# Performance work log

Measured on AMD Instinct MI355X. Metric: run time of the kernel, lower is better.

The kernel has to match this reference:

```python
import jax, jax.numpy as jnp
import numpy as np

N = 8192   # nodes
F = 16     # node features (col 0 = signal, last 3 = xyz)
H = 64     # hidden
G = 256    # number of graphs (segments)
EPS = 1e-3 # keras LayerNormalization default epsilon


def setup_inputs() -> dict:
    key = jax.random.key(0)
    ks = jax.random.split(key, 10)
    s = 0.05
    X = jax.random.normal(ks[0], (N, F), jnp.float32)
    # dense pre-normalized adjacency (spektral GCNConv expects normalized A)
    A = jax.random.uniform(ks[1], (N, N), jnp.float32) * (1.0 / N)
    I = jnp.sort(jax.random.randint(ks[2], (N,), 0, G)).astype(jnp.int32)
    W0 = jax.random.normal(ks[3], (F, H), jnp.float32) * s
    b0 = jnp.zeros((H,), jnp.float32)
    g0 = jnp.ones((H,), jnp.float32)
    be0 = jnp.zeros((H,), jnp.float32)
    W1 = jax.random.normal(ks[4], (H, H), jnp.float32) * s
    b1 = jnp.zeros((H,), jnp.float32)
    g1 = jnp.ones((H,), jnp.float32)
    be1 = jnp.zeros((H,), jnp.float32)
    Wf = jax.random.normal(ks[5], (H, H), jnp.float32) * s
    bf = jnp.zeros((H,), jnp.float32)
    Wa = jax.random.normal(ks[6], (H, H), jnp.float32) * s
    ba = jnp.zeros((H,), jnp.float32)
    Wout = jax.random.normal(ks[7], (H + 3, 3), jnp.float32) * s
    bout = jnp.zeros((3,), jnp.float32)
    return dict(X=X, A=A, I=I, W0=W0, b0=b0, g0=g0, be0=be0,
                W1=W1, b1=b1, g1=g1, be1=be1,
                Wf=Wf, bf=bf, Wa=Wa, ba=ba, Wout=Wout, bout=bout)


def _layer_norm(x, gamma, beta):
    m = jnp.mean(x, axis=-1, keepdims=True)
    v = jnp.mean(jnp.square(x - m), axis=-1, keepdims=True)
    return (x - m) * jax.lax.rsqrt(v + EPS) * gamma + beta


def reference(X, A, I, W0, b0, g0, be0, W1, b1, g1, be1, Wf, bf, Wa, ba, Wout, bout):
    I = I.astype(jnp.int32)
    # GCN layer 0: relu(A @ X @ W0 + b0) -> LayerNorm
    h0 = _layer_norm(jax.nn.relu(A @ (X @ W0) + b0), g0, be0)
    # GCN layer 1 + LayerNorm + residual (i > 0)
    h = _layer_norm(jax.nn.relu(A @ (h0 @ W1) + b1), g1, be1) + h0
    # GlobalAttentionPool: Dense features * sigmoid-gated attention, segment-summed per graph
    feat = h @ Wf + bf                       # [N, H]
    attn = jax.nn.sigmoid(h @ Wa + ba)       # [N, H]
    g = jax.ops.segment_sum(feat * attn, I, num_segments=G)  # [G, H]
    # Signal-weighted barycentre via segment-softmax over log1p(relu(signal))
    z = jnp.log1p(jax.nn.relu(X[:, 0]))                       # [N]
    zmax = jax.ops.segment_max(z, I, num_segments=G)          # [G]
    zexp = jnp.exp(z - zmax[I])                               # [N]
    zsum = jax.ops.segment_sum(zexp, I, num_segments=G)       # [G]
    w = zexp / zsum[I]                                        # [N]
    bary = jax.ops.segment_sum(w[:, None] * X[:, -3:], I, num_segments=G)  # [G, 3]
    return jnp.concatenate([g, bary], axis=-1) @ Wout + bout  # [G, 3]
```

## Files before the change

kernel.cpp:

```cpp
#include <hip/hip_runtime.h>
#include <hip/hip_bf16.h>
#include <math.h>

#define NN 8192
#define FF 16
#define HH 64
#define GG 256
#define LN_EPS 1e-3f
#define KSPLIT 8
#define KC (NN / KSPLIT)

typedef __bf16 bf16x8 __attribute__((ext_vector_type(8)));
typedef float  floatx4 __attribute__((ext_vector_type(4)));

__global__ void k1_xw0(const float* __restrict__ X,
                       const float* __restrict__ W0,
                       const int* __restrict__ I,
                       __hip_bfloat16* __restrict__ Zt0,
                       float* __restrict__ zarr,
                       unsigned int* __restrict__ zmax_bits) {
    const int b = blockIdx.x, tid = threadIdx.x;
    const int lane = tid & 63;
    const int i = (b & 127) * 64 + lane;
    const int n = ((b >> 7) << 2) + (tid >> 6);
    float s = 0.f;
#pragma unroll
    for (int m = 0; m < FF; ++m)
        s += X[i * FF + m] * W0[m * HH + n];
    Zt0[(size_t)n * NN + i] = __float2bfloat16(s);

    if (b < 128 && tid < 64) {
        const int ii = b * 64 + lane;
        float z = log1pf(fmaxf(X[ii * FF], 0.f));
        zarr[ii] = z;
        atomicMax(&zmax_bits[I[ii]], __float_as_uint(z));
    }
}

__global__ __launch_bounds__(256)
void k_gemm_split(const float* __restrict__ A,
                  const __hip_bfloat16* __restrict__ Zt,
                  float* __restrict__ C) {
    const int tid  = threadIdx.x;
    const int wave = tid >> 6;
    const int lane = tid & 63;
    const int l16  = lane & 15;
    const int quad = lane >> 4;
    const int rb   = blockIdx.x & 127;
    const int kb   = blockIdx.x >> 7;
    const int row0 = rb * 64;
    const int k0   = kb * KC;

    const float* aptr = A + (size_t)(row0 + wave * 16 + l16) * NN + k0 + quad * 8;
    const __hip_bfloat16* bp0 = Zt + (size_t)(0 * 16 + l16) * NN + k0 + quad * 8;
    const __hip_bfloat16* bp1 = Zt + (size_t)(1 * 16 + l16) * NN + k0 + quad * 8;
    const __hip_bfloat16* bp2 = Zt + (size_t)(2 * 16 + l16) * NN + k0 + quad * 8;
    const __hip_bfloat16* bp3 = Zt + (size_t)(3 * 16 + l16) * NN + k0 + quad * 8;

    floatx4 acc0 = {0.f,0.f,0.f,0.f}, acc1 = {0.f,0.f,0.f,0.f};
    floatx4 acc2 = {0.f,0.f,0.f,0.f}, acc3 = {0.f,0.f,0.f,0.f};

#pragma unroll 4
    for (int k = 0; k < KC; k += 32) {
        const float4 a0 = *reinterpret_cast<const float4*>(aptr + k);
        const float4 a1 = *reinterpret_cast<const float4*>(aptr + k + 4);
        bf16x8 af;
        af[0] = (__bf16)a0.x; af[1] = (__bf16)a0.y;
        af[2] = (__bf16)a0.z; af[3] = (__bf16)a0.w;
        af[4] = (__bf16)a1.x; af[5] = (__bf16)a1.y;
        af[6] = (__bf16)a1.z; af[7] = (__bf16)a1.w;
        const bf16x8 b0 = *reinterpret_cast<const bf16x8*>(bp0 + k);
        const bf16x8 b1 = *reinterpret_cast<const bf16x8*>(bp1 + k);
        const bf16x8 b2 = *reinterpret_cast<const bf16x8*>(bp2 + k);
        const bf16x8 b3 = *reinterpret_cast<const bf16x8*>(bp3 + k);
        acc0 = __builtin_amdgcn_mfma_f32_16x16x32_bf16(af, b0, acc0, 0, 0, 0);
        acc1 = __builtin_amdgcn_mfma_f32_16x16x32_bf16(af, b1, acc1, 0, 0, 0);
        acc2 = __builtin_amdgcn_mfma_f32_16x16x32_bf16(af, b2, acc2, 0, 0, 0);
        acc3 = __builtin_amdgcn_mfma_f32_16x16x32_bf16(af, b3, acc3, 0, 0, 0);
    }

    const size_t rbase = (size_t)(row0 + wave * 16 + quad * 4);
#pragma unroll
    for (int r = 0; r < 4; ++r) {
        float* crow = C + (rbase + r) * HH + l16;
        atomicAdd(crow +  0, acc0[r]);
        atomicAdd(crow + 16, acc1[r]);
        atomicAdd(crow + 32, acc2[r]);
        atomicAdd(crow + 48, acc3[r]);
    }
}

__global__ __launch_bounds__(256)
void k_ln(const float* __restrict__ C,
          const float* __restrict__ bias,
          const float* __restrict__ gamma,
          const float* __restrict__ beta,
          const float* __restrict__ resid,
          float* __restrict__ out) {
    const int tid = threadIdx.x;
    const int row = tid >> 4;
    const int c0  = (tid & 15) * 4;
    const size_t grow = (size_t)(blockIdx.x * 16 + row);

    float4 v4 = *reinterpret_cast<const float4*>(&C[grow * HH + c0]);
    const float4 b4 = *reinterpret_cast<const float4*>(&bias[c0]);
    float v[4] = { fmaxf(v4.x + b4.x, 0.f), fmaxf(v4.y + b4.y, 0.f),
                   fmaxf(v4.z + b4.z, 0.f), fmaxf(v4.w + b4.w, 0.f) };
    float s = 0.f, ss = 0.f;
#pragma unroll
    for (int j = 0; j < 4; ++j) { s += v[j]; ss += v[j] * v[j]; }
#pragma unroll
    for (int m = 1; m < 16; m <<= 1) {
        s  += __shfl_xor(s,  m, 64);
        ss += __shfl_xor(ss, m, 64);
    }
    const float mean = s * (1.f / 64.f);
    const float var  = fmaxf(ss * (1.f / 64.f) - mean * mean, 0.f);
    const float inv  = rsqrtf(var + LN_EPS);
    const float4 g4  = *reinterpret_cast<const float4*>(&gamma[c0]);
    const float4 be4 = *reinterpret_cast<const float4*>(&beta[c0]);
    float4 o;
    o.x = (v[0] - mean) * inv * g4.x + be4.x;
    o.y = (v[1] - mean) * inv * g4.y + be4.y;
    o.z = (v[2] - mean) * inv * g4.z + be4.z;
    o.w = (v[3] - mean) * inv * g4.w + be4.w;
    if (resid) {
        const float4 r4 = *reinterpret_cast<const float4*>(&resid[grow * HH + c0]);
        o.x += r4.x; o.y += r4.y; o.z += r4.z; o.w += r4.w;
    }
    *reinterpret_cast<float4*>(&out[grow * HH + c0]) = o;
}

__global__ void k3_hw1(const float* __restrict__ h0,
                       const float* __restrict__ W1,
                       __hip_bfloat16* __restrict__ Zt1) {
    const int b = blockIdx.x, tid = threadIdx.x;
    const int lane = tid & 63;
    const int i = (b & 127) * 64 + lane;
    const int n = ((b >> 7) << 2) + (tid >> 6);
    float s = 0.f;
#pragma unroll 8
    for (int m = 0; m < HH; ++m)
        s += h0[(size_t)i * HH + m] * W1[m * HH + n];
    Zt1[(size_t)n * NN + i] = __float2bfloat16(s);
}

__global__ __launch_bounds__(256)
void k5_pool(const float* __restrict__ h,
             const float* __restrict__ Wf, const float* __restrict__ bfv,
             const float* __restrict__ Wa, const float* __restrict__ bav,
             const int* __restrict__ I,
             float* __restrict__ g) {
    __shared__ float hrow[4][64];
    const int w = threadIdx.x >> 6, l = threadIdx.x & 63;
    const int node = blockIdx.x * 4 + w;
    hrow[w][l] = h[(size_t)node * HH + l];
    __syncthreads();
    float sf = bfv[l], sa = bav[l];
#pragma unroll 8
    for (int m = 0; m < HH; ++m) {
        const float hv = hrow[w][m];
        sf += hv * Wf[m * HH + l];
        sa += hv * Wa[m * HH + l];
    }
    const float attn = 1.f / (1.f + expf(-sa));
    atomicAdd(&g[(size_t)I[node] * HH + l], sf * attn);
}

__global__ void k6_bary(const float* __restrict__ X,
                        const int* __restrict__ I,
                        const float* __restrict__ zarr,
                        const float* __restrict__ zmax,
                        float* __restrict__ zsum,
                        float* __restrict__ baryn) {
    const int i = blockIdx.x * 256 + threadIdx.x;
    const int seg = I[i];
    const float ze = expf(zarr[i] - zmax[seg]);
    atomicAdd(&zsum[seg], ze);
    atomicAdd(&baryn[seg * 3 + 0], ze * X[i * FF + 13]);
    atomicAdd(&baryn[seg * 3 + 1], ze * X[i * FF + 14]);
    atomicAdd(&baryn[seg * 3 + 2], ze * X[i * FF + 15]);
}

__global__ void k7_out(const float* __restrict__ g,
                       const float* __restrict__ zsum,
                       const float* __restrict__ baryn,
                       const float* __restrict__ Wout,
                       const float* __restrict__ bout,
                       float* __restrict__ out) {
    const int w = threadIdx.x >> 6, lane = threadIdx.x & 63;
    const int gi = blockIdx.x * 4 + w;
    const float vg = g[(size_t)gi * HH + lane];
    const float zs = zsum[gi];
    const float invz = (zs > 0.f) ? (1.f / zs) : 0.f;
    const float extra = (lane < 3) ? baryn[gi * 3 + lane] * invz : 0.f;
#pragma unroll
    for (int d = 0; d < 3; ++d) {
        float p = vg * Wout[lane * 3 + d];
        if (lane < 3) p += extra * Wout[(64 + lane) * 3 + d];
#pragma unroll
        for (int m = 1; m < 64; m <<= 1) p += __shfl_xor(p, m, 64);
        if (lane == 0) out[gi * 3 + d] = p + bout[d];
    }
}

extern "C" void kernel_launch(void* const* d_in, const int* in_sizes, int n_in,
                              void* d_out, int out_size, void* d_ws, size_t ws_size,
                              hipStream_t stream) {
    const float* X   = (const float*)d_in[0];
    const float* A   = (const float*)d_in[1];
    const int*   I   = (const int*)d_in[2];
    const float* W0  = (const float*)d_in[3];
    const float* b0  = (const float*)d_in[4];
    const float* g0  = (const float*)d_in[5];
    const float* be0 = (const float*)d_in[6];
    const float* W1  = (const float*)d_in[7];
    const float* b1  = (const float*)d_in[8];
    const float* g1  = (const float*)d_in[9];
    const float* be1 = (const float*)d_in[10];
    const float* Wf  = (const float*)d_in[11];
    const float* bfv = (const float*)d_in[12];
    const float* Wa  = (const float*)d_in[13];
    const float* bav = (const float*)d_in[14];
    const float* Wo  = (const float*)d_in[15];
    const float* bo  = (const float*)d_in[16];

    char* ws = (char*)d_ws;
    float* C0   = (float*)(ws);
    float* C1   = (float*)(ws + (2u << 20));
    float* accr = (float*)(ws + (4u << 20));
    float* g     = accr;
    float* zmax  = accr + GG * HH;
    float* zsum  = zmax + GG;
    float* baryn = zsum + GG;
    const size_t memset_bytes = (size_t)(2 * NN * HH + GG * HH + GG + GG + GG * 3) * sizeof(float);

    __hip_bfloat16* Zt0 = (__hip_bfloat16*)(ws + (4u << 20) + (128u << 10));
    __hip_bfloat16* Zt1 = (__hip_bfloat16*)(ws + (5u << 20) + (128u << 10));
    float* h0   = (float*)(ws + (6u << 20) + (128u << 10));
    float* h    = (float*)(ws + (8u << 20) + (128u << 10));
    float* zarr = (float*)(ws + (10u << 20) + (128u << 10));

    hipMemsetAsync(ws, 0, memset_bytes, stream);

    k1_xw0<<<2048, 256, 0, stream>>>(X, W0, I, Zt0, zarr, (unsigned int*)zmax);
    k_gemm_split<<<1024, 256, 0, stream>>>(A, Zt0, C0);
    k_ln<<<512, 256, 0, stream>>>(C0, b0, g0, be0, nullptr, h0);
    k3_hw1<<<2048, 256, 0, stream>>>(h0, W1, Zt1);
    k_gemm_split<<<1024, 256, 0, stream>>>(A, Zt1, C1);
    k_ln<<<512, 256, 0, stream>>>(C1, b1, g1, be1, h0, h);
    k5_pool<<<2048, 256, 0, stream>>>(h, Wf, bfv, Wa, bav, I, g);
    k6_bary<<<32, 256, 0, stream>>>(X, I, zarr, zmax, zsum, baryn);
    k7_out<<<64, 256, 0, stream>>>(g, zsum, baryn, Wo, bo, (float*)d_out);
}
```

Before: 602.0 us.

## Replace split-K atomics with partial buffers, tile small GEMMs in LDS, fuse bary into pool

The split-K GEMM now writes per-split partial results to a dedicated buffer, and the LayerNorm kernel sums them, which removes the float atomics and most of the memset. KSPLIT doubles to 16. The X@W0 and h0@W1 kernels are rewritten to stage tiles in shared memory, with each thread computing 16 outputs. The barycentre segment sums are folded into the pooling kernel, which drops a launch. The cost is writing and re-reading 16 partial buffers of 2 MB each per layer, and the reduction order changes.

```diff
diff --git a/kernel.cpp b/kernel.cpp
--- a/kernel.cpp
+++ b/kernel.cpp
@@ -7,40 +7,62 @@
 #define HH 64
 #define GG 256
 #define LN_EPS 1e-3f
-#define KSPLIT 8
+#define KSPLIT 16
 #define KC (NN / KSPLIT)
 
 typedef __bf16 bf16x8 __attribute__((ext_vector_type(8)));
 typedef float  floatx4 __attribute__((ext_vector_type(4)));
 
-__global__ void k1_xw0(const float* __restrict__ X,
-                       const float* __restrict__ W0,
-                       const int* __restrict__ I,
-                       __hip_bfloat16* __restrict__ Zt0,
-                       float* __restrict__ zarr,
-                       unsigned int* __restrict__ zmax_bits) {
-    const int b = blockIdx.x, tid = threadIdx.x;
-    const int lane = tid & 63;
-    const int i = (b & 127) * 64 + lane;
-    const int n = ((b >> 7) << 2) + (tid >> 6);
-    float s = 0.f;
-#pragma unroll
-    for (int m = 0; m < FF; ++m)
-        s += X[i * FF + m] * W0[m * HH + n];
-    Zt0[(size_t)n * NN + i] = __float2bfloat16(s);
-
-    if (b < 128 && tid < 64) {
-        const int ii = b * 64 + lane;
-        float z = log1pf(fmaxf(X[ii * FF], 0.f));
-        zarr[ii] = z;
-        atomicMax(&zmax_bits[I[ii]], __float_as_uint(z));
+__global__ __launch_bounds__(256)
+void k1_xw0(const float* __restrict__ X,
+            const float* __restrict__ W0,
+            const int* __restrict__ I,
+            __hip_bfloat16* __restrict__ Zt0,
+            float* __restrict__ zarr,
+            unsigned int* __restrict__ zmax_bits) {
+    __shared__ float Xs[64][17];
+    __shared__ float W0s[16][64];
+    const int t  = threadIdx.x;
+    const int i0 = blockIdx.x * 64;
+    {
+        const int r = t >> 2, c = (t & 3) * 4;
+        const float4 v = *reinterpret_cast<const float4*>(&X[(size_t)(i0 + r) * FF + c]);
+        Xs[r][c + 0] = v.x; Xs[r][c + 1] = v.y; Xs[r][c + 2] = v.z; Xs[r][c + 3] = v.w;
+        const float4 w = *reinterpret_cast<const float4*>(&W0[t * 4]);
+        const int wr = t >> 4, wc = (t & 15) * 4;
+        W0s[wr][wc + 0] = w.x; W0s[wr][wc + 1] = w.y; W0s[wr][wc + 2] = w.z; W0s[wr][wc + 3] = w.w;
+    }
+    __syncthreads();
+    const int i  = t & 63;
+    const int n0 = (t >> 6) * 16;
+    float s[16];
+#pragma unroll
+    for (int j = 0; j < 16; ++j) s[j] = 0.f;
+#pragma unroll
+    for (int m = 0; m < FF; ++m) {
+        const float hv = Xs[i][m];
+        const float4* wrow = reinterpret_cast<const float4*>(&W0s[m][n0]);
+        const float4 w0 = wrow[0], w1 = wrow[1], w2 = wrow[2], w3 = wrow[3];
+        s[0]  += hv * w0.x; s[1]  += hv * w0.y; s[2]  += hv * w0.z; s[3]  += hv * w0.w;
+        s[4]  += hv * w1.x; s[5]  += hv * w1.y; s[6]  += hv * w1.z; s[7]  += hv * w1.w;
+        s[8]  += hv * w2.x; s[9]  += hv * w2.y; s[10] += hv * w2.z; s[11] += hv * w2.w;
+        s[12] += hv * w3.x; s[13] += hv * w3.y; s[14] += hv * w3.z; s[15] += hv * w3.w;
+    }
+#pragma unroll
+    for (int j = 0; j < 16; ++j)
+        Zt0[(size_t)(n0 + j) * NN + i0 + i] = __float2bfloat16(s[j]);
+
+    if (t < 64) {
+        const float z = log1pf(fmaxf(Xs[t][0], 0.f));
+        zarr[i0 + t] = z;
+        atomicMax(&zmax_bits[I[i0 + t]], __float_as_uint(z));
     }
 }
 
 __global__ __launch_bounds__(256)
 void k_gemm_split(const float* __restrict__ A,
                   const __hip_bfloat16* __restrict__ Zt,
-                  float* __restrict__ C) {
+                  float* __restrict__ Cp) {
     const int tid  = threadIdx.x;
     const int wave = tid >> 6;
     const int lane = tid & 63;
@@ -79,33 +101,37 @@
         acc3 = __builtin_amdgcn_mfma_f32_16x16x32_bf16(af, b3, acc3, 0, 0, 0);
     }
 
-    const size_t rbase = (size_t)(row0 + wave * 16 + quad * 4);
+    float* cp = Cp + ((size_t)kb * NN + row0 + wave * 16 + quad * 4) * HH + l16;
 #pragma unroll
     for (int r = 0; r < 4; ++r) {
-        float* crow = C + (rbase + r) * HH + l16;
-        atomicAdd(crow +  0, acc0[r]);
-        atomicAdd(crow + 16, acc1[r]);
-        atomicAdd(crow + 32, acc2[r]);
-        atomicAdd(crow + 48, acc3[r]);
-    }
-}
-
-__global__ __launch_bounds__(256)
-void k_ln(const float* __restrict__ C,
-          const float* __restrict__ bias,
-          const float* __restrict__ gamma,
-          const float* __restrict__ beta,
-          const float* __restrict__ resid,
-          float* __restrict__ out) {
+        cp[(size_t)r * HH +  0] = acc0[r];
+        cp[(size_t)r * HH + 16] = acc1[r];
+        cp[(size_t)r * HH + 32] = acc2[r];
+        cp[(size_t)r * HH + 48] = acc3[r];
+    }
+}
+
+__global__ __launch_bounds__(256)
+void k_red_ln(const float* __restrict__ Cp,
+              const float* __restrict__ bias,
+              const float* __restrict__ gamma,
+              const float* __restrict__ beta,
+              const float* __restrict__ resid,
+              float* __restrict__ out) {
     const int tid = threadIdx.x;
     const int row = tid >> 4;
     const int c0  = (tid & 15) * 4;
     const size_t grow = (size_t)(blockIdx.x * 16 + row);
 
-    float4 v4 = *reinterpret_cast<const float4*>(&C[grow * HH + c0]);
+    float4 a = {0.f, 0.f, 0.f, 0.f};
+#pragma unroll
+    for (int kb = 0; kb < KSPLIT; ++kb) {
+        const float4 v = *reinterpret_cast<const float4*>(&Cp[((size_t)kb * NN + grow) * HH + c0]);
+        a.x += v.x; a.y += v.y; a.z += v.z; a.w += v.w;
+    }
     const float4 b4 = *reinterpret_cast<const float4*>(&bias[c0]);
-    float v[4] = { fmaxf(v4.x + b4.x, 0.f), fmaxf(v4.y + b4.y, 0.f),
-                   fmaxf(v4.z + b4.z, 0.f), fmaxf(v4.w + b4.w, 0.f) };
+    float v[4] = { fmaxf(a.x + b4.x, 0.f), fmaxf(a.y + b4.y, 0.f),
+                   fmaxf(a.z + b4.z, 0.f), fmaxf(a.w + b4.w, 0.f) };
     float s = 0.f, ss = 0.f;
 #pragma unroll
     for (int j = 0; j < 4; ++j) { s += v[j]; ss += v[j] * v[j]; }
@@ -131,18 +157,42 @@
     *reinterpret_cast<float4*>(&out[grow * HH + c0]) = o;
 }
 
-__global__ void k3_hw1(const float* __restrict__ h0,
-                       const float* __restrict__ W1,
-                       __hip_bfloat16* __restrict__ Zt1) {
-    const int b = blockIdx.x, tid = threadIdx.x;
-    const int lane = tid & 63;
-    const int i = (b & 127) * 64 + lane;
-    const int n = ((b >> 7) << 2) + (tid >> 6);
-    float s = 0.f;
-#pragma unroll 8
-    for (int m = 0; m < HH; ++m)
-        s += h0[(size_t)i * HH + m] * W1[m * HH + n];
-    Zt1[(size_t)n * NN + i] = __float2bfloat16(s);
+__global__ __launch_bounds__(256)
+void k3_hw1(const float* __restrict__ h0,
+            const float* __restrict__ W1,
+            __hip_bfloat16* __restrict__ Zt1) {
+    __shared__ float Hs[64][65];
+    __shared__ float Ws[64][64];
+    const int t  = threadIdx.x;
+    const int i0 = blockIdx.x * 64;
+#pragma unroll
+    for (int p = 0; p < 4; ++p) {
+        const int idx = p * 256 + t;
+        const int r = idx >> 4, c = (idx & 15) * 4;
+        const float4 v = *reinterpret_cast<const float4*>(&h0[(size_t)(i0 + r) * HH + c]);
+        Hs[r][c + 0] = v.x; Hs[r][c + 1] = v.y; Hs[r][c + 2] = v.z; Hs[r][c + 3] = v.w;
+        const float4 w = *reinterpret_cast<const float4*>(&W1[(size_t)r * HH + c]);
+        Ws[r][c + 0] = w.x; Ws[r][c + 1] = w.y; Ws[r][c + 2] = w.z; Ws[r][c + 3] = w.w;
+    }
+    __syncthreads();
+    const int i  = t & 63;
+    const int n0 = (t >> 6) * 16;
+    float s[16];
+#pragma unroll
+    for (int j = 0; j < 16; ++j) s[j] = 0.f;
+#pragma unroll
+    for (int m = 0; m < HH; ++m) {
+        const float hv = Hs[i][m];
+        const float4* wrow = reinterpret_cast<const float4*>(&Ws[m][n0]);
+        const float4 w0 = wrow[0], w1 = wrow[1], w2 = wrow[2], w3 = wrow[3];
+        s[0]  += hv * w0.x; s[1]  += hv * w0.y; s[2]  += hv * w0.z; s[3]  += hv * w0.w;
+        s[4]  += hv * w1.x; s[5]  += hv * w1.y; s[6]  += hv * w1.z; s[7]  += hv * w1.w;
+        s[8]  += hv * w2.x; s[9]  += hv * w2.y; s[10] += hv * w2.z; s[11] += hv * w2.w;
+        s[12] += hv * w3.x; s[13] += hv * w3.y; s[14] += hv * w3.z; s[15] += hv * w3.w;
+    }
+#pragma unroll
+    for (int j = 0; j < 16; ++j)
+        Zt1[(size_t)(n0 + j) * NN + i0 + i] = __float2bfloat16(s[j]);
 }
 
 __global__ __launch_bounds__(256)
@@ -150,7 +200,12 @@
              const float* __restrict__ Wf, const float* __restrict__ bfv,
              const float* __restrict__ Wa, const float* __restrict__ bav,
              const int* __restrict__ I,
-             float* __restrict__ g) {
+             const float* __restrict__ X,
+             const float* __restrict__ zarr,
+             const float* __restrict__ zmax,
+             float* __restrict__ g,
+             float* __restrict__ zsum,
+             float* __restrict__ baryn) {
     __shared__ float hrow[4][64];
     const int w = threadIdx.x >> 6, l = threadIdx.x & 63;
     const int node = blockIdx.x * 4 + w;
@@ -164,30 +219,23 @@
         sa += hv * Wa[m * HH + l];
     }
     const float attn = 1.f / (1.f + expf(-sa));
-    atomicAdd(&g[(size_t)I[node] * HH + l], sf * attn);
-}
-
-__global__ void k6_bary(const float* __restrict__ X,
-                        const int* __restrict__ I,
-                        const float* __restrict__ zarr,
-                        const float* __restrict__ zmax,
-                        float* __restrict__ zsum,
-                        float* __restrict__ baryn) {
-    const int i = blockIdx.x * 256 + threadIdx.x;
-    const int seg = I[i];
-    const float ze = expf(zarr[i] - zmax[seg]);
-    atomicAdd(&zsum[seg], ze);
-    atomicAdd(&baryn[seg * 3 + 0], ze * X[i * FF + 13]);
-    atomicAdd(&baryn[seg * 3 + 1], ze * X[i * FF + 14]);
-    atomicAdd(&baryn[seg * 3 + 2], ze * X[i * FF + 15]);
-}
-
-__global__ void k7_out(const float* __restrict__ g,
-                       const float* __restrict__ zsum,
-                       const float* __restrict__ baryn,
-                       const float* __restrict__ Wout,
-                       const float* __restrict__ bout,
-                       float* __restrict__ out) {
+    const int seg = I[node];
+    atomicAdd(&g[(size_t)seg * HH + l], sf * attn);
+
+    if (l < 4) {
+        const float ze = expf(zarr[node] - zmax[seg]);
+        if (l == 0) atomicAdd(&zsum[seg], ze);
+        else        atomicAdd(&baryn[seg * 3 + (l - 1)], ze * X[(size_t)node * FF + 12 + l]);
+    }
+}
+
+__global__ __launch_bounds__(256)
+void k7_out(const float* __restrict__ g,
+            const float* __restrict__ zsum,
+            const float* __restrict__ baryn,
+            const float* __restrict__ Wout,
+            const float* __restrict__ bout,
+            float* __restrict__ out) {
     const int w = threadIdx.x >> 6, lane = threadIdx.x & 63;
     const int gi = blockIdx.x * 4 + w;
     const float vg = g[(size_t)gi * HH + lane];
@@ -226,30 +274,27 @@
     const float* bo  = (const float*)d_in[16];
 
     char* ws = (char*)d_ws;
-    float* C0   = (float*)(ws);
-    float* C1   = (float*)(ws + (2u << 20));
-    float* accr = (float*)(ws + (4u << 20));
-    float* g     = accr;
-    float* zmax  = accr + GG * HH;
+    float* Cp = (float*)ws;
+    __hip_bfloat16* Zt0 = (__hip_bfloat16*)(ws + (32u << 20));
+    __hip_bfloat16* Zt1 = (__hip_bfloat16*)(ws + (33u << 20));
+    float* h0   = (float*)(ws + (34u << 20));
+    float* h    = (float*)(ws + (36u << 20));
+    float* zarr = (float*)(ws + (38u << 20));
+    float* acc  = (float*)(ws + (38u << 20) + (64u << 10));
+    float* g     = acc;
+    float* zmax  = acc + GG * HH;
     float* zsum  = zmax + GG;
     float* baryn = zsum + GG;
-    const size_t memset_bytes = (size_t)(2 * NN * HH + GG * HH + GG + GG + GG * 3) * sizeof(float);
-
-    __hip_bfloat16* Zt0 = (__hip_bfloat16*)(ws + (4u << 20) + (128u << 10));
-    __hip_bfloat16* Zt1 = (__hip_bfloat16*)(ws + (5u << 20) + (128u << 10));
-    float* h0   = (float*)(ws + (6u << 20) + (128u << 10));
-    float* h    = (float*)(ws + (8u << 20) + (128u << 10));
-    float* zarr = (float*)(ws + (10u << 20) + (128u << 10));
-
-    hipMemsetAsync(ws, 0, memset_bytes, stream);
-
-    k1_xw0<<<2048, 256, 0, stream>>>(X, W0, I, Zt0, zarr, (unsigned int*)zmax);
-    k_gemm_split<<<1024, 256, 0, stream>>>(A, Zt0, C0);
-    k_ln<<<512, 256, 0, stream>>>(C0, b0, g0, be0, nullptr, h0);
-    k3_hw1<<<2048, 256, 0, stream>>>(h0, W1, Zt1);
-    k_gemm_split<<<1024, 256, 0, stream>>>(A, Zt1, C1);
-    k_ln<<<512, 256, 0, stream>>>(C1, b1, g1, be1, h0, h);
-    k5_pool<<<2048, 256, 0, stream>>>(h, Wf, bfv, Wa, bav, I, g);
-    k6_bary<<<32, 256, 0, stream>>>(X, I, zarr, zmax, zsum, baryn);
+    const size_t memset_bytes = (size_t)(GG * HH + GG + GG + GG * 3) * sizeof(float);
+
+    hipMemsetAsync(acc, 0, memset_bytes, stream);
+
+    k1_xw0<<<128, 256, 0, stream>>>(X, W0, I, Zt0, zarr, (unsigned int*)zmax);
+    k_gemm_split<<<2048, 256, 0, stream>>>(A, Zt0, Cp);
+    k_red_ln<<<512, 256, 0, stream>>>(Cp, b0, g0, be0, nullptr, h0);
+    k3_hw1<<<128, 256, 0, stream>>>(h0, W1, Zt1);
+    k_gemm_split<<<2048, 256, 0, stream>>>(A, Zt1, Cp);
+    k_red_ln<<<512, 256, 0, stream>>>(Cp, b1, g1, be1, h0, h);
+    k5_pool<<<2048, 256, 0, stream>>>(h, Wf, bfv, Wa, bav, I, X, zarr, zmax, g, zsum, baryn);
     k7_out<<<64, 256, 0, stream>>>(g, zsum, baryn, Wo, bo, (float*)d_out);
 }
```

New measurement: 582.6 us. 3.2% less time.
